# Kernel optimization log

Measured on AMD Instinct MI355X. Metric: run time of the kernel, lower is better.

Reference implementation:

```python
import jax, jax.numpy as jnp
import numpy as np

N, E = 50000, 800000          # nodes, edges
IN, H, OUT = 256, 128, 2       # input feat, hidden_channels, out_channels
NEG_SLOPE = 0.2                # GATv2 LeakyReLU slope (PyG default)


def _w(key, fan_in, fan_out):
    return jax.random.normal(key, (fan_in, fan_out), jnp.float32) / np.sqrt(fan_in).astype(np.float32)


def setup_inputs() -> dict:
    key = jax.random.key(0)
    ks = jax.random.split(key, 24)
    inp = {
        "x": jax.random.normal(ks[0], (N, IN), jnp.float32),
        "edge_index": jax.random.randint(ks[1], (2, E), 0, N, jnp.int32),
        # GATv2Conv 0: in=IN -> H
        "c0_Wl": _w(ks[2], IN, H), "c0_Wr": _w(ks[3], IN, H),
        "c0_att": jax.random.normal(ks[4], (H,), jnp.float32) / np.sqrt(H).astype(np.float32),
        "c0_b": jnp.zeros((H,), jnp.float32),
        # GATv2Conv 1: H -> H
        "c1_Wl": _w(ks[5], H, H), "c1_Wr": _w(ks[6], H, H),
        "c1_att": jax.random.normal(ks[7], (H,), jnp.float32) / np.sqrt(H).astype(np.float32),
        "c1_b": jnp.zeros((H,), jnp.float32),
        # final GATv2Conv: H -> OUT
        "cf_Wl": _w(ks[8], H, OUT), "cf_Wr": _w(ks[9], H, OUT),
        "cf_att": jax.random.normal(ks[10], (OUT,), jnp.float32) / np.sqrt(OUT).astype(np.float32),
        "cf_b": jnp.zeros((OUT,), jnp.float32),
        # residual Linears
        "l0_W": _w(ks[11], IN, H), "l0_b": jnp.zeros((H,), jnp.float32),
        "l1_W": _w(ks[12], H, H), "l1_b": jnp.zeros((H,), jnp.float32),
        "lf_W": _w(ks[13], H, OUT), "lf_b": jnp.zeros((OUT,), jnp.float32),
    }
    return inp


def gatv2(x, edge_index, Wl, Wr, att, bias):
    """PyG GATv2Conv, heads=1, add_self_loops=False, share_weights=False."""
    src, dst = edge_index[0], edge_index[1]
    xs = x @ Wl                                   # [N,H] source transform
    xd = x @ Wr                                   # [N,H] target transform
    h = jax.nn.leaky_relu(xs[src] + xd[dst], NEG_SLOPE)   # [E,H]
    e = h @ att                                   # [E] attention logits
    # segment softmax over incoming edges of each destination node
    m = jax.ops.segment_max(e, dst, num_segments=N)
    m = jnp.where(jnp.isfinite(m), m, 0.0)
    p = jnp.exp(e - m[dst])
    s = jax.ops.segment_sum(p, dst, num_segments=N)
    alpha = p / (s[dst] + 1e-16)                  # [E]
    out = jax.ops.segment_sum(alpha[:, None] * xs[src], dst, num_segments=N)
    return out + bias


def reference(x, edge_index, c0_Wl, c0_Wr, c0_att, c0_b, c1_Wl, c1_Wr, c1_att, c1_b,
              cf_Wl, cf_Wr, cf_att, cf_b, l0_W, l0_b, l1_W, l1_b, lf_W, lf_b):
    # layer 0 + residual linear, then ReLU
    h = gatv2(x, edge_index, c0_Wl, c0_Wr, c0_att, c0_b) + (jax.nn.relu(x) @ l0_W + l0_b)
    h = jax.nn.relu(h)
    # layer 1 -> embeddings
    emb = gatv2(h, edge_index, c1_Wl, c1_Wr, c1_att, c1_b) + (jax.nn.relu(h) @ l1_W + l1_b)
    # final layer -> logits
    out = gatv2(emb, edge_index, cf_Wl, cf_Wr, cf_att, cf_b) + (jax.nn.relu(emb) @ lf_W + lf_b)
    return (out, emb)
```

## Files before the change

kernel.cpp:

```cpp
#include <hip/hip_runtime.h>
#include <hip/hip_bf16.h>

#define NEG_SLOPE 0.2f

typedef __attribute__((ext_vector_type(8))) _Float16 half8;
typedef __attribute__((ext_vector_type(2))) _Float16 h2v;
typedef __attribute__((ext_vector_type(4))) float f32x4;

__device__ __forceinline__ float toF(float x) { return x; }
__device__ __forceinline__ float toF(__hip_bfloat16 x) { return __bfloat162float(x); }
__device__ __forceinline__ float toF(_Float16 x) { return (float)x; }

__device__ __forceinline__ void stT(float* p, size_t i, float v) { p[i] = v; }
__device__ __forceinline__ void stT(__hip_bfloat16* p, size_t i, float v) {
    p[i] = __float2bfloat16(v);
}
__device__ __forceinline__ void stT(_Float16* p, size_t i, float v) { p[i] = (_Float16)v; }

template <typename T> struct IsBF { static constexpr bool v = false; };
template <> struct IsBF<__hip_bfloat16> { static constexpr bool v = true; };

__device__ __forceinline__ void vwaitn(int n) {
    if (n == 0) asm volatile("s_waitcnt vmcnt(0)" ::: "memory");
    else if (n == 7) asm volatile("s_waitcnt vmcnt(7)" ::: "memory");
    else if (n == 8) asm volatile("s_waitcnt vmcnt(8)" ::: "memory");
    else if (n == 9) asm volatile("s_waitcnt vmcnt(9)" ::: "memory");
    else asm volatile("s_waitcnt vmcnt(10)" ::: "memory");
}

__global__ void k_detect(const unsigned* __restrict__ x, int* __restrict__ flag) {
    unsigned u = x[threadIdx.x];
    int lo_exp = (int)((u >> 7) & 0xFFu);
    int ok = (lo_exp >= 90 && lo_exp <= 141) ? 1 : 0;
    unsigned long long b = __ballot(ok);
    if (threadIdx.x == 0) flag[0] = (__popcll(b) >= 48) ? 1 : 0;
}

__global__ __launch_bounds__(256) void k_cnt(const int* __restrict__ src,
                                             const int* __restrict__ dst, int E,
                                             int* __restrict__ gcnt,
                                             unsigned* __restrict__ bbuf, int cap) {
    __shared__ int hist[64];
    __shared__ int lbase[64];
    __shared__ int gbase[64];
    __shared__ int lfill[64];
    __shared__ unsigned ebuf[4096];
    __shared__ unsigned char bb[4096];
    int t = threadIdx.x;
    int e0 = blockIdx.x * 4096;
    if (t < 64) { hist[t] = 0; lfill[t] = 0; }
    __syncthreads();
    unsigned my[16];
    int mybkt[16];
#pragma unroll
    for (int i = 0; i < 16; ++i) {
        int idx = e0 + i * 256 + t;
        if (idx < E) {
            int d = dst[idx];
            int b = d >> 10;
            mybkt[i] = b;
            my[i] = (unsigned)src[idx] | ((unsigned)(d & 1023) << 16);
            atomicAdd(&hist[b], 1);
        } else {
            mybkt[i] = -1;
        }
    }
    __syncthreads();
    if (t < 64) {
        int h = hist[t];
        int v = h;
#pragma unroll
        for (int o = 1; o < 64; o <<= 1) {
            int u = __shfl_up(v, o, 64);
            if (t >= o) v += u;
        }
        lbase[t] = v - h;
        gbase[t] = (h > 0) ? atomicAdd(&gcnt[t], h) : 0;
    }
    __syncthreads();
#pragma unroll
    for (int i = 0; i < 16; ++i) {
        int b = mybkt[i];
        if (b >= 0) {
            int p = lbase[b] + atomicAdd(&lfill[b], 1);
            ebuf[p] = my[i];
            bb[p] = (unsigned char)b;
        }
    }
    __syncthreads();
    int total = min(4096, E - e0);
    for (int p = t; p < total; p += 256) {
        int b = bb[p];
        int o = gbase[b] + (p - lbase[b]);
        if (o < cap) bbuf[(size_t)b * cap + o] = ebuf[p];
    }
}

__global__ void k_bbase(const int* __restrict__ gcnt, int* __restrict__ bbase, int nb,
                        int cap) {
    int t = threadIdx.x;
    int c = (t < nb) ? min(gcnt[t], cap) : 0;
    int v = c;
#pragma unroll
    for (int o = 1; o < 64; o <<= 1) {
        int u = __shfl_up(v, o, 64);
        if (t >= o) v += u;
    }
    if (t < nb) bbase[t] = v - c;
}

__global__ __launch_bounds__(256) void k_bhp(const int* __restrict__ gcnt,
                                             const int* __restrict__ bbase,
                                             const unsigned* __restrict__ bbuf, int cap,
                                             int* __restrict__ rowptr,
                                             int* __restrict__ csr_src, int n, int nb) {
    __shared__ int hist[1024];
    __shared__ int fill[1024];
    __shared__ int wsum[4];
    int b = blockIdx.x, t = threadIdx.x, lane = t & 63, w = t >> 6;
    for (int i = t; i < 1024; i += 256) { hist[i] = 0; fill[i] = 0; }
    __syncthreads();
    int cnt = min(gcnt[b], cap);
    const unsigned* p = bbuf + (size_t)b * cap;
    for (int i = t; i < cnt; i += 256) atomicAdd(&hist[p[i] >> 16], 1);
    __syncthreads();
    int base0 = bbase[b];
    int idx = t * 4;
    int c0 = hist[idx + 0], c1 = hist[idx + 1], c2 = hist[idx + 2], c3 = hist[idx + 3];
    int s1 = c0 + c1, s2 = s1 + c2, s3 = s2 + c3;
    int v = s3;
#pragma unroll
    for (int o = 1; o < 64; o <<= 1) {
        int u = __shfl_up(v, o, 64);
        if (lane >= o) v += u;
    }
    if (lane == 63) wsum[w] = v;
    __syncthreads();
    int woff = 0;
#pragma unroll
    for (int i = 0; i < 3; ++i)
        if (i < w) woff += wsum[i];
    int excl = base0 + woff + v - s3;
    hist[idx + 0] = excl;
    hist[idx + 1] = excl + c0;
    hist[idx + 2] = excl + s1;
    hist[idx + 3] = excl + s2;
    int d0 = b * 1024 + idx;
#pragma unroll
    for (int i = 0; i < 4; ++i)
        if (d0 + i < n) rowptr[d0 + i] = hist[idx + i];
    if (b == nb - 1 && t == 255) rowptr[n] = base0 + cnt;
    __syncthreads();
    for (int i = t; i < cnt; i += 256) {
        unsigned e = p[i];
        int dl = (int)(e >> 16);
        int pos = hist[dl] + atomicAdd(&fill[dl], 1);
        csr_src[pos] = (int)(e & 0xFFFFu);
    }
}

__global__ void k_hist(const int* __restrict__ dst, int E, int* __restrict__ rowptr) {
    int i = blockIdx.x * blockDim.x + threadIdx.x;
    if (i < E) atomicAdd(&rowptr[dst[i] + 1], 1);
}

__global__ void k_scatter(const int* __restrict__ src, const int* __restrict__ dst, int E,
                          const int* __restrict__ rowptr, int* __restrict__ fill,
                          int* __restrict__ csr_src) {
    int i = blockIdx.x * blockDim.x + threadIdx.x;
    if (i < E) {
        int d = dst[i];
        int pos = rowptr[d] + atomicAdd(&fill[d], 1);
        csr_src[pos] = src[i];
    }
}

__global__ __launch_bounds__(256) void k_scan1(int* __restrict__ rowptr,
                                               int* __restrict__ blksum, int n) {
    __shared__ int wsum[4];
    int t = threadIdx.x, lane = t & 63, w = t >> 6;
    int idx = blockIdx.x * 1024 + t * 4;
    int c0 = (idx + 0 < n) ? rowptr[idx + 1] : 0;
    int c1 = (idx + 1 < n) ? rowptr[idx + 2] : 0;
    int c2 = (idx + 2 < n) ? rowptr[idx + 3] : 0;
    int c3 = (idx + 3 < n) ? rowptr[idx + 4] : 0;
    int s1 = c0 + c1, s2 = s1 + c2, s3 = s2 + c3;
    int v = s3;
#pragma unroll
    for (int o = 1; o < 64; o <<= 1) {
        int u = __shfl_up(v, o, 64);
        if (lane >= o) v += u;
    }
    if (lane == 63) wsum[w] = v;
    __syncthreads();
    int woff = 0;
#pragma unroll
    for (int i = 0; i < 3; ++i)
        if (i < w) woff += wsum[i];
    int excl = woff + v - s3;
    if (idx + 0 < n) rowptr[idx + 1] = excl + c0;
    if (idx + 1 < n) rowptr[idx + 2] = excl + s1;
    if (idx + 2 < n) rowptr[idx + 3] = excl + s2;
    if (idx + 3 < n) rowptr[idx + 4] = excl + s3;
    if (t == 255) blksum[blockIdx.x] = woff + v;
}

__global__ void k_scan2(int* __restrict__ blksum, int nblk) {
    int t = threadIdx.x;
    int v = (t < nblk) ? blksum[t] : 0;
#pragma unroll
    for (int o = 1; o < 64; o <<= 1) {
        int u = __shfl_up(v, o, 64);
        if (t >= o) v += u;
    }
    if (t < nblk) blksum[t] = v;
}

__global__ void k_scan3(int* __restrict__ rowptr, const int* __restrict__ blksum, int n) {
    int idx = blockIdx.x * blockDim.x + threadIdx.x;
    if (idx < n) {
        int b = idx >> 10;
        if (b > 0) rowptr[idx + 1] += blksum[b - 1];
    }
}

template <typename WT>
__device__ void packW_body(const WT* W0, const WT* W1, const WT* W2, const WT* b2, int K,
                           _Float16* Bp, float* biasf) {
    int lane = threadIdx.x;
    int ksteps = K >> 5;
    int nb = 3 * ksteps * 8;
    int bid = blockIdx.x;
    if (bid == nb) {
        biasf[lane * 2 + 0] = toF(b2[lane * 2 + 0]);
        biasf[lane * 2 + 1] = toF(b2[lane * 2 + 1]);
        return;
    }
    int ks = bid / 24;
    int rem = bid - ks * 24;
    int o = rem >> 3, ct = rem & 7;
    const WT* W = (o == 0) ? W0 : ((o == 1) ? W1 : W2);
    int c = ct * 16 + (lane & 15);
    int k0 = ks * 32 + (lane >> 4) * 8;
    _Float16* out = Bp + (size_t)bid * 512 + lane * 8;
#pragma unroll
    for (int i = 0; i < 8; ++i) out[i] = (_Float16)toF(W[(size_t)(k0 + i) * 128 + c]);
}

__global__ void k_packW(const int* __restrict__ flag, const void* W0, const void* W1,
                        const void* W2, const void* b2, int K, _Float16* __restrict__ Bp,
                        float* __restrict__ biasf) {
    if (flag[0] == 0)
        packW_body<float>((const float*)W0, (const float*)W1, (const float*)W2,
                          (const float*)b2, K, Bp, biasf);
    else
        packW_body<__hip_bfloat16>((const __hip_bfloat16*)W0, (const __hip_bfloat16*)W1,
                                   (const __hip_bfloat16*)W2, (const __hip_bfloat16*)b2, K,
                                   Bp, biasf);
}

template <typename AT, typename O2T, int KSTEPS>
__device__ void gemm_body(const AT* __restrict__ A, int N,
                          const _Float16* __restrict__ Bp, const float* __restrict__ biasf,
                          _Float16* __restrict__ O0, _Float16* __restrict__ O1,
                          O2T* __restrict__ O2, _Float16 (*sB)[12288]) {
    const int H = 128;
    const int K = KSTEPS * 32;
    int tid = threadIdx.x;
    int wave = tid >> 6, lane = tid & 63;
    int row0 = (blockIdx.x * 4 + wave) * 16;
    int rr = lane & 15, kg = lane >> 4;
    int arow = min(row0 + rr, N - 1);
    constexpr int NR = (sizeof(AT) == 4) ? 2 : 1;

    f32x4 acc[3][8];
#pragma unroll
    for (int o = 0; o < 3; ++o)
#pragma unroll
        for (int ct = 0; ct < 8; ++ct) acc[o][ct] = f32x4{0.f, 0.f, 0.f, 0.f};

    auto stage = [&](int b, int ksv) {
        const char* gsrc = (const char*)(Bp + (size_t)ksv * 12288) + wave * 1024 + lane * 16;
        char* lbase = (char*)(&sB[b][0]) + wave * 1024;
#pragma unroll
        for (int r = 0; r < 6; ++r) {
            __builtin_amdgcn_global_load_lds(
                (const __attribute__((address_space(1))) unsigned*)(gsrc + r * 4096),
                (__attribute__((address_space(3))) unsigned*)(lbase + r * 4096), 16, 0, 0);
        }
    };
    auto loadA = [&](int ksv, uint4* dst) {
        const char* p = (const char*)A + ((size_t)arow * K + ksv * 32 + kg * 8) * sizeof(AT);
        dst[0] = *(const uint4*)p;
        if constexpr (NR == 2) dst[1] = *(const uint4*)(p + 16);
    };
    auto compute = [&](const uint4* raw, const _Float16* sb) {
        half8 a0, a1, r0f, r1f;
        if constexpr (sizeof(AT) == 4) {
            union { uint4 u[2]; float f[8]; } cv;
            cv.u[0] = raw[0]; cv.u[1] = raw[1];
#pragma unroll
            for (int i = 0; i < 8; ++i) {
                float a = cv.f[i];
                _Float16 h = (_Float16)a;
                float lof = a - (float)h;
                _Float16 lo = (_Float16)lof;
                bool pos = a > 0.f;
                a0[i] = h; a1[i] = lo;
                r0f[i] = pos ? h : (_Float16)0.f;
                r1f[i] = pos ? lo : (_Float16)0.f;
            }
        } else if constexpr (IsBF<AT>::v) {
            union { uint4 u4; unsigned u[4]; } cv;
            cv.u4 = raw[0];
#pragma unroll
            for (int q = 0; q < 4; ++q) {
                union { unsigned u; float f; } lo, hi;
                lo.u = cv.u[q] << 16;
                hi.u = cv.u[q] & 0xFFFF0000u;
                a0[2 * q] = (_Float16)lo.f;
                a0[2 * q + 1] = (_Float16)hi.f;
                r0f[2 * q] = (_Float16)fmaxf(lo.f, 0.f);
                r0f[2 * q + 1] = (_Float16)fmaxf(hi.f, 0.f);
            }
        } else {
            union { uint4 u4; half8 h; } cv;
            cv.u4 = raw[0];
            a0 = cv.h;
#pragma unroll
            for (int i = 0; i < 8; ++i)
                r0f[i] = (a0[i] > (_Float16)0.f) ? a0[i] : (_Float16)0.f;
        }
#pragma unroll
        for (int ct = 0; ct < 8; ++ct) {
            half8 w0 = *(const half8*)(sb + (0 * 8 + ct) * 512 + lane * 8);
            half8 w1 = *(const half8*)(sb + (1 * 8 + ct) * 512 + lane * 8);
            half8 w2 = *(const half8*)(sb + (2 * 8 + ct) * 512 + lane * 8);
            acc[0][ct] = __builtin_amdgcn_mfma_f32_16x16x32_f16(a0, w0, acc[0][ct], 0, 0, 0);
            acc[1][ct] = __builtin_amdgcn_mfma_f32_16x16x32_f16(a0, w1, acc[1][ct], 0, 0, 0);
            acc[2][ct] = __builtin_amdgcn_mfma_f32_16x16x32_f16(r0f, w2, acc[2][ct], 0, 0, 0);
            if constexpr (sizeof(AT) == 4) {
                acc[0][ct] = __builtin_amdgcn_mfma_f32_16x16x32_f16(a1, w0, acc[0][ct], 0, 0, 0);
                acc[1][ct] = __builtin_amdgcn_mfma_f32_16x16x32_f16(a1, w1, acc[1][ct], 0, 0, 0);
                acc[2][ct] = __builtin_amdgcn_mfma_f32_16x16x32_f16(r1f, w2, acc[2][ct], 0, 0, 0);
            }
        }
    };

    uint4 rA[3][NR];
    loadA(0, rA[0]);
    loadA(1, rA[1]);
    stage(0, 0);
#pragma unroll
    for (int ks = 0; ks < KSTEPS; ++ks) {
        if (ks + 1 < KSTEPS) {
            stage((ks + 1) & 1, ks + 1);
            asm volatile("" ::: "memory");
        }
        if (ks + 2 < KSTEPS) loadA(ks + 2, rA[(ks + 2) % 3]);
        if (ks == 0 || ks == KSTEPS - 2) vwaitn(NR + 6);
        else if (ks + 2 < KSTEPS) vwaitn(2 * NR + 6);
        else vwaitn(0);
        __builtin_amdgcn_s_barrier();
        compute(rA[ks % 3], &sB[ks & 1][0]);
        __builtin_amdgcn_s_barrier();
    }

    int rb = row0 + kg * 4;
#pragma unroll
    for (int ct = 0; ct < 8; ++ct) {
        int c = ct * 16 + rr;
        float bv = biasf[c];
#pragma unroll
        for (int j = 0; j < 4; ++j) {
            int row = rb + j;
            if (row < N) {
                size_t o = (size_t)row * H + c;
                O0[o] = (_Float16)acc[0][ct][j];
                O1[o] = (_Float16)acc[1][ct][j];
                stT(O2, o, acc[2][ct][j] + bv);
            }
        }
    }
}

template <int LAYER>
__global__ __launch_bounds__(256) void gemm3_u(const int* __restrict__ flag, const void* Aext,
                                               const _Float16* Af16, int N,
                                               const _Float16* __restrict__ Bp,
                                               const float* __restrict__ biasf,
                                               _Float16* __restrict__ O0,
                                               _Float16* __restrict__ O1, _Float16* O2h,
                                               float* O2f, __hip_bfloat16* O2b) {
    __shared__ _Float16 sB[2][12288];
    int f = flag[0];
    if constexpr (LAYER == 0) {
        if (f == 0)
            gemm_body<float, _Float16, 8>((const float*)Aext, N, Bp, biasf, O0, O1, O2h, sB);
        else
            gemm_body<__hip_bfloat16, _Float16, 8>((const __hip_bfloat16*)Aext, N, Bp, biasf,
                                                   O0, O1, O2h, sB);
    } else {
        if (f == 0)
            gemm_body<_Float16, float, 4>(Af16, N, Bp, biasf, O0, O1, O2f, sB);
        else
            gemm_body<_Float16, __hip_bfloat16, 4>(Af16, N, Bp, biasf, O0, O1, O2b, sB);
    }
}

template <typename IOT, typename T, int FINAL>
__device__ void gat_body(const _Float16* __restrict__ xs, const _Float16* __restrict__ xd,
                         const int* __restrict__ rowptr, const int* __restrict__ csr_src,
                         IOT* __restrict__ io, const T* __restrict__ att,
                         const T* __restrict__ gbias, int n, int relu_out,
                         const T* __restrict__ Wl, const T* __restrict__ Wr,
                         const T* __restrict__ Wres, const T* __restrict__ bres,
                         float* __restrict__ xsf, float* __restrict__ xdf,
                         float* __restrict__ resf) {
    int tid = threadIdx.x;
    int l = tid & 15;
    int g = tid >> 4;
    int dst = blockIdx.x * 16 + g;
    if (blockIdx.x * 16 + ((tid >> 6) << 2) >= n) return;
    int dstc = min(dst, n - 1);
    bool act = dst < n;

    union U4H { uint4 u; h2v h[4]; };
    U4H du; du.u = *(const uint4*)(xd + (size_t)dstc * 128 + l * 8);
    h2v ap[4];
#pragma unroll
    for (int c = 0; c < 4; ++c) {
        ap[c][0] = (_Float16)toF(att[l * 8 + 2 * c]);
        ap[c][1] = (_Float16)toF(att[l * 8 + 2 * c + 1]);
    }
    const _Float16 ks = (_Float16)NEG_SLOPE;
    const h2v k02 = {ks, ks};

    int beg = rowptr[dstc];
    int end = act ? rowptr[dstc + 1] : beg;
    float m = -INFINITY, s = 0.f;
    h2v acc[4];
#pragma unroll
    for (int c = 0; c < 4; ++c) acc[c] = h2v{(_Float16)0.f, (_Float16)0.f};

    auto GATHER = [&](U4H (&v)[8], int j0) {
#pragma unroll
        for (int q = 0; q < 8; ++q) {
            int idx = j0 + q;
            if (idx >= end) idx = j0;
            int sq = csr_src[idx];
            v[q].u = *(const uint4*)(xs + (size_t)sq * 128 + l * 8);
        }
    };
    auto COMPUTE = [&](U4H (&v)[8], int j0) {
        int rem = end - j0;
        float p[8];
#pragma unroll
        for (int q = 0; q < 8; ++q) p[q] = 0.f;
#pragma unroll
        for (int c = 0; c < 4; ++c) {
#pragma unroll
            for (int q = 0; q < 8; ++q) {
                h2v t = v[q].h[c] + du.h[c];
                t = __builtin_elementwise_max(t, t * k02);
                p[q] = __builtin_amdgcn_fdot2(t, ap[c], p[q], false);
            }
        }
#pragma unroll
        for (int o = 1; o < 16; o <<= 1) {
#pragma unroll
            for (int q = 0; q < 8; ++q) p[q] += __shfl_xor(p[q], o, 16);
        }
#pragma unroll
        for (int q = 1; q < 8; ++q)
            if (rem < q + 1) p[q] = -INFINITY;
        float pm = p[0];
#pragma unroll
        for (int q = 1; q < 8; ++q) pm = fmaxf(pm, p[q]);
        float nm = fmaxf(m, pm);
        float sc = __expf(m - nm);
        float w[8];
        float ws = 0.f;
#pragma unroll
        for (int q = 0; q < 8; ++q) {
            w[q] = __expf(p[q] - nm);
            ws += w[q];
        }
        s = s * sc + ws;
        _Float16 sch = (_Float16)sc;
        h2v scp = {sch, sch};
        h2v wp[8];
#pragma unroll
        for (int q = 0; q < 8; ++q) {
            _Float16 wh = (_Float16)w[q];
            wp[q] = h2v{wh, wh};
        }
#pragma unroll
        for (int c = 0; c < 4; ++c) {
            h2v a = acc[c] * scp;
#pragma unroll
            for (int q = 0; q < 8; ++q) a = a + v[q].h[c] * wp[q];
            acc[c] = a;
        }
        m = nm;
    };

    U4H va[8], vb[8];
    if (beg < end) GATHER(va, beg);
    for (int j = beg; j < end; j += 16) {
        if (j + 8 < end) GATHER(vb, j + 8);
        COMPUTE(va, j);
        if (j + 8 < end) {
            if (j + 16 < end) GATHER(va, j + 16);
            COMPUTE(vb, j + 8);
        }
    }

    if (act) {
        float r = 1.f / (s + 1e-16f);
        size_t base = (size_t)dst * 128 + l * 8;
        float ev[8];
#pragma unroll
        for (int c = 0; c < 4; ++c) {
            int f0 = l * 8 + 2 * c;
            float v0 = (float)acc[c][0] * r + toF(gbias[f0]) + toF(io[base + 2 * c]);
            float v1 = (float)acc[c][1] * r + toF(gbias[f0 + 1]) + toF(io[base + 2 * c + 1]);
            if (relu_out) { v0 = fmaxf(v0, 0.f); v1 = fmaxf(v1, 0.f); }
            stT(io, base + 2 * c, v0);
            stT(io, base + 2 * c + 1, v1);
            ev[2 * c] = v0;
            ev[2 * c + 1] = v1;
        }
        if constexpr (FINAL) {
            float d[6] = {0.f, 0.f, 0.f, 0.f, 0.f, 0.f};
#pragma unroll
            for (int f = 0; f < 8; ++f) {
                int fg = (l * 8 + f) * 2;
                float e = ev[f];
                float rp = fmaxf(e, 0.f);
                d[0] += e * toF(Wl[fg]);
                d[1] += e * toF(Wl[fg + 1]);
                d[2] += e * toF(Wr[fg]);
                d[3] += e * toF(Wr[fg + 1]);
                d[4] += rp * toF(Wres[fg]);
                d[5] += rp * toF(Wres[fg + 1]);
            }
#pragma unroll
            for (int i = 0; i < 6; ++i) {
#pragma unroll
                for (int o = 1; o < 16; o <<= 1) d[i] += __shfl_xor(d[i], o, 16);
            }
            if (l == 0) {
                xsf[dst * 2 + 0] = d[0];
                xsf[dst * 2 + 1] = d[1];
                xdf[dst * 2 + 0] = d[2];
                xdf[dst * 2 + 1] = d[3];
                resf[dst * 2 + 0] = d[4] + toF(bres[0]);
                resf[dst * 2 + 1] = d[5] + toF(bres[1]);
            }
        }
    }
}

template <int FINAL>
__global__ __launch_bounds__(256) void gat_u(const int* __restrict__ flag,
                                             const _Float16* __restrict__ xs,
                                             const _Float16* __restrict__ xd,
                                             const int* __restrict__ rowptr,
                                             const int* __restrict__ csr_src, _Float16* io_h,
                                             float* io_f, __hip_bfloat16* io_b, const void* att,
                                             const void* gbias, int n, int relu_out,
                                             const void* Wl, const void* Wr, const void* Wres,
                                             const void* bres, float* xsf, float* xdf,
                                             float* resf) {
    typedef __hip_bfloat16 bf;
    int f = flag[0];
    if constexpr (FINAL == 0) {
        if (f == 0)
            gat_body<_Float16, float, 0>(xs, xd, rowptr, csr_src, io_h, (const float*)att,
                                         (const float*)gbias, n, relu_out, nullptr, nullptr,
                                         nullptr, nullptr, nullptr, nullptr, nullptr);
        else
            gat_body<_Float16, bf, 0>(xs, xd, rowptr, csr_src, io_h, (const bf*)att,
                                      (const bf*)gbias, n, relu_out, nullptr, nullptr, nullptr,
                                      nullptr, nullptr, nullptr, nullptr);
    } else {
        if (f == 0)
            gat_body<float, float, 1>(xs, xd, rowptr, csr_src, io_f, (const float*)att,
                                      (const float*)gbias, n, relu_out, (const float*)Wl,
                                      (const float*)Wr, (const float*)Wres, (const float*)bres,
                                      xsf, xdf, resf);
        else
            gat_body<bf, bf, 1>(xs, xd, rowptr, csr_src, io_b, (const bf*)att, (const bf*)gbias,
                                n, relu_out, (const bf*)Wl, (const bf*)Wr, (const bf*)Wres,
                                (const bf*)bres, xsf, xdf, resf);
    }
}

template <typename T>
__device__ void fe_body(const float* __restrict__ xsf, const float* __restrict__ xdf,
                        const float* __restrict__ resf, const int* __restrict__ rowptr,
                        const int* __restrict__ csr_src, const T* __restrict__ att,
                        const T* __restrict__ gb, T* __restrict__ out, int n) {
    int dst = blockIdx.x * blockDim.x + threadIdx.x;
    if (dst >= n) return;
    float2 dv = ((const float2*)xdf)[dst];
    float a0 = toF(att[0]), a1 = toF(att[1]);
    float m = -INFINITY, s = 0.f, acc0 = 0.f, acc1 = 0.f;
    int beg = rowptr[dst], end = rowptr[dst + 1];
    for (int j = beg; j < end; j += 4) {
        int rem = end - j;
        int i1 = (rem > 1) ? 1 : 0, i2 = (rem > 2) ? 2 : 0, i3 = (rem > 3) ? 3 : 0;
        int s0 = csr_src[j];
        int s1 = csr_src[j + i1];
        int s2 = csr_src[j + i2];
        int s3 = csr_src[j + i3];
        float2 v0 = ((const float2*)xsf)[s0];
        float2 v1 = ((const float2*)xsf)[s1];
        float2 v2 = ((const float2*)xsf)[s2];
        float2 v3 = ((const float2*)xsf)[s3];
        float h0, h1, e0, e1, e2, e3;
        h0 = v0.x + dv.x; h0 = fmaxf(h0, NEG_SLOPE * h0);
        h1 = v0.y + dv.y; h1 = fmaxf(h1, NEG_SLOPE * h1);
        e0 = h0 * a0 + h1 * a1;
        h0 = v1.x + dv.x; h0 = fmaxf(h0, NEG_SLOPE * h0);
        h1 = v1.y + dv.y; h1 = fmaxf(h1, NEG_SLOPE * h1);
        e1 = h0 * a0 + h1 * a1;
        h0 = v2.x + dv.x; h0 = fmaxf(h0, NEG_SLOPE * h0);
        h1 = v2.y + dv.y; h1 = fmaxf(h1, NEG_SLOPE * h1);
        e2 = h0 * a0 + h1 * a1;
        h0 = v3.x + dv.x; h0 = fmaxf(h0, NEG_SLOPE * h0);
        h1 = v3.y + dv.y; h1 = fmaxf(h1, NEG_SLOPE * h1);
        e3 = h0 * a0 + h1 * a1;
        if (rem < 2) e1 = -INFINITY;
        if (rem < 3) e2 = -INFINITY;
        if (rem < 4) e3 = -INFINITY;
        float pm = fmaxf(fmaxf(e0, e1), fmaxf(e2, e3));
        float nm = fmaxf(m, pm);
        float sc = __expf(m - nm);
        float w0 = __expf(e0 - nm), w1 = __expf(e1 - nm);
        float w2 = __expf(e2 - nm), w3 = __expf(e3 - nm);
        s = s * sc + ((w0 + w1) + (w2 + w3));
        acc0 = acc0 * sc + ((w0 * v0.x + w1 * v1.x) + (w2 * v2.x + w3 * v3.x));
        acc1 = acc1 * sc + ((w0 * v0.y + w1 * v1.y) + (w2 * v2.y + w3 * v3.y));
        m = nm;
    }
    float r = 1.f / (s + 1e-16f);
    float2 rv = ((const float2*)resf)[dst];
    stT(out, (size_t)dst * 2 + 0, acc0 * r + toF(gb[0]) + rv.x);
    stT(out, (size_t)dst * 2 + 1, acc1 * r + toF(gb[1]) + rv.y);
}

__global__ void final_edge_u(const int* __restrict__ flag, const float* __restrict__ xsf,
                             const float* __restrict__ xdf, const float* __restrict__ resf,
                             const int* __restrict__ rowptr, const int* __restrict__ csr_src,
                             const void* att, const void* gb, void* out, int n) {
    typedef __hip_bfloat16 bf;
    if (flag[0] == 0)
        fe_body<float>(xsf, xdf, resf, rowptr, csr_src, (const float*)att, (const float*)gb,
                       (float*)out, n);
    else
        fe_body<bf>(xsf, xdf, resf, rowptr, csr_src, (const bf*)att, (const bf*)gb, (bf*)out, n);
}

extern "C" void kernel_launch(void* const* d_in, const int* in_sizes, int n_in,
                              void* d_out, int out_size, void* d_ws, size_t ws_size,
                              hipStream_t stream) {
    typedef __hip_bfloat16 bf;
    typedef _Float16 f16;
    const int IN = 256, H = 128;
    const int N = in_sizes[0] / IN;
    const int E = in_sizes[1] / 2;

    const int* ei = (const int*)d_in[1];

    size_t off = 0;
    auto alloc = [&](size_t bytes) {
        void* p = (char*)d_ws + off;
        off += (bytes + 255) & ~(size_t)255;
        return p;
    };
    f16* xs = (f16*)alloc((size_t)N * H * 2);
    f16* xd = (f16*)alloc((size_t)N * H * 2);
    f16* hb = (f16*)alloc((size_t)N * H * 2);
    int* flag = (int*)alloc(256);
    int* rowptr = (int*)alloc((size_t)(N + 1) * 4);
    int* fill = (int*)alloc((size_t)N * 4);
    int* blksum = (int*)alloc(256 * 4);
    int* csr_src = (int*)alloc((size_t)E * 4);
    float* xsf = (float*)alloc((size_t)N * 2 * 4);
    float* xdf = (float*)alloc((size_t)N * 2 * 4);
    float* resf = (float*)alloc((size_t)N * 2 * 4);
    f16* Bp0 = (f16*)alloc((size_t)3 * 8 * 8 * 512 * 2);
    f16* Bp1 = (f16*)alloc((size_t)3 * 4 * 8 * 512 * 2);
    float* bias0 = (float*)alloc(128 * 4);
    float* bias1 = (float*)alloc(128 * 4);
    const int NB = (N + 1023) / 1024;
    const int CAP = ((2 * (E / (NB > 0 ? NB : 1) + 1) + 255) / 256) * 256;
    int* gcnt = (int*)alloc(64 * 4);
    int* bbase = (int*)alloc(64 * 4);
    unsigned* bbuf = (unsigned*)alloc((size_t)NB * CAP * 4);

    const int* e_src = ei;
    const int* e_dst = ei + E;

    k_detect<<<1, 64, 0, stream>>>((const unsigned*)d_in[0], flag);
    if (N <= 65536) {
        hipMemsetAsync(gcnt, 0, 64 * 4, stream);
        k_cnt<<<(E + 4095) / 4096, 256, 0, stream>>>(e_src, e_dst, E, gcnt, bbuf, CAP);
        k_bbase<<<1, 64, 0, stream>>>(gcnt, bbase, NB, CAP);
        k_bhp<<<NB, 256, 0, stream>>>(gcnt, bbase, bbuf, CAP, rowptr, csr_src, N, NB);
    } else {
        const int nblk = (N + 1023) / 1024;
        hipMemsetAsync(rowptr, 0, (size_t)(N + 1) * 4, stream);
        hipMemsetAsync(fill, 0, (size_t)N * 4, stream);
        k_hist<<<(E + 255) / 256, 256, 0, stream>>>(e_dst, E, rowptr);
        k_scan1<<<nblk, 256, 0, stream>>>(rowptr, blksum, N);
        k_scan2<<<1, 64, 0, stream>>>(blksum, nblk);
        k_scan3<<<(N + 255) / 256, 256, 0, stream>>>(rowptr, blksum, N);
        k_scatter<<<(E + 255) / 256, 256, 0, stream>>>(e_src, e_dst, E, rowptr, fill, csr_src);
    }

    k_packW<<<3 * 8 * 8 + 1, 64, 0, stream>>>(flag, d_in[2], d_in[3], d_in[14], d_in[15], IN,
                                              Bp0, bias0);
    k_packW<<<3 * 4 * 8 + 1, 64, 0, stream>>>(flag, d_in[6], d_in[7], d_in[16], d_in[17], H,
                                              Bp1, bias1);

    const int g64 = (N + 63) / 64;
    const int eblk16 = (N + 15) / 16;

    float* embF = (float*)d_out + (size_t)N * 2;
    bf* embB = (bf*)d_out + (size_t)N * 2;

    gemm3_u<0><<<g64, 256, 0, stream>>>(flag, d_in[0], nullptr, N, Bp0, bias0, xs, xd, hb,
                                        nullptr, nullptr);
    gat_u<0><<<eblk16, 256, 0, stream>>>(flag, xs, xd, rowptr, csr_src, hb, nullptr, nullptr,
                                         d_in[4], d_in[5], N, 1, nullptr, nullptr, nullptr,
                                         nullptr, nullptr, nullptr, nullptr);

    gemm3_u<1><<<g64, 256, 0, stream>>>(flag, nullptr, hb, N, Bp1, bias1, xs, xd, nullptr,
                                        embF, embB);
    gat_u<1><<<eblk16, 256, 0, stream>>>(flag, xs, xd, rowptr, csr_src, nullptr, embF, embB,
                                         d_in[8], d_in[9], N, 0, d_in[10], d_in[11], d_in[18],
                                         d_in[19], xsf, xdf, resf);

    final_edge_u<<<(N + 255) / 256, 256, 0, stream>>>(flag, xsf, xdf, resf, rowptr, csr_src,
                                                      d_in[12], d_in[13], d_out, N);
}
```

Baseline: 325.0 us.

## Merge preprocessing launches and co-schedule edge bucketing with layer-0 GEMM

Merges dtype detection, gcnt zeroing and both weight-packing launches into one prep kernel. The edge bucket-count pass now runs in the same launch as the layer-0 GEMM (mega0), with blocks split by index. The bucket-base scan is folded into k_bhp, and the gather loop's double-buffered software pipeline is replaced by a simple single-buffer loop. The aim is fewer kernel launches and memset calls, plus overlapping CSR construction with GEMM work. Dropping the prefetch pipelining in the aggregation may expose more memory latency, and the shared 48KB dynamic shared memory can limit occupancy for the count blocks.

```diff
diff --git a/kernel.cpp b/kernel.cpp
--- a/kernel.cpp
+++ b/kernel.cpp
@@ -28,26 +28,82 @@
     else asm volatile("s_waitcnt vmcnt(10)" ::: "memory");
 }
 
-__global__ void k_detect(const unsigned* __restrict__ x, int* __restrict__ flag) {
-    unsigned u = x[threadIdx.x];
+__device__ __forceinline__ int detect_local(const unsigned* __restrict__ x, int t) {
+    unsigned u = x[t];
     int lo_exp = (int)((u >> 7) & 0xFFu);
     int ok = (lo_exp >= 90 && lo_exp <= 141) ? 1 : 0;
     unsigned long long b = __ballot(ok);
-    if (threadIdx.x == 0) flag[0] = (__popcll(b) >= 48) ? 1 : 0;
-}
-
-__global__ __launch_bounds__(256) void k_cnt(const int* __restrict__ src,
-                                             const int* __restrict__ dst, int E,
+    return (__popcll(b) >= 48) ? 1 : 0;
+}
+
+template <typename WT>
+__device__ void packW_body(const WT* W0, const WT* W1, const WT* W2, const WT* b2, int K,
+                           _Float16* Bp, float* biasf, int bid) {
+    int lane = threadIdx.x;
+    int ksteps = K >> 5;
+    int nb = 3 * ksteps * 8;
+    if (bid == nb) {
+        biasf[lane * 2 + 0] = toF(b2[lane * 2 + 0]);
+        biasf[lane * 2 + 1] = toF(b2[lane * 2 + 1]);
+        return;
+    }
+    int ks = bid / 24;
+    int rem = bid - ks * 24;
+    int o = rem >> 3, ct = rem & 7;
+    const WT* W = (o == 0) ? W0 : ((o == 1) ? W1 : W2);
+    int c = ct * 16 + (lane & 15);
+    int k0 = ks * 32 + (lane >> 4) * 8;
+    _Float16* out = Bp + (size_t)bid * 512 + lane * 8;
+#pragma unroll
+    for (int i = 0; i < 8; ++i) out[i] = (_Float16)toF(W[(size_t)(k0 + i) * 128 + c]);
+}
+
+__global__ __launch_bounds__(64) void k_prep(const unsigned* __restrict__ x, int* __restrict__ flag,
                                              int* __restrict__ gcnt,
-                                             unsigned* __restrict__ bbuf, int cap) {
-    __shared__ int hist[64];
-    __shared__ int lbase[64];
-    __shared__ int gbase[64];
-    __shared__ int lfill[64];
-    __shared__ unsigned ebuf[4096];
-    __shared__ unsigned char bb[4096];
+                                             const void* W0a, const void* W1a, const void* W2a,
+                                             const void* b2a, const void* W0b, const void* W1b,
+                                             const void* W2b, const void* b2b,
+                                             _Float16* __restrict__ Bp0, float* __restrict__ bias0,
+                                             _Float16* __restrict__ Bp1, float* __restrict__ bias1) {
+    typedef __hip_bfloat16 bf;
     int t = threadIdx.x;
-    int e0 = blockIdx.x * 4096;
+    int f = detect_local(x, t);
+    int bid = blockIdx.x;
+    if (bid == 0) {
+        if (t == 0) flag[0] = f;
+        gcnt[t] = 0;
+        return;
+    }
+    bid -= 1;
+    if (bid < 193) {
+        if (f == 0)
+            packW_body<float>((const float*)W0a, (const float*)W1a, (const float*)W2a,
+                              (const float*)b2a, 256, Bp0, bias0, bid);
+        else
+            packW_body<bf>((const bf*)W0a, (const bf*)W1a, (const bf*)W2a, (const bf*)b2a, 256,
+                           Bp0, bias0, bid);
+    } else {
+        bid -= 193;
+        if (f == 0)
+            packW_body<float>((const float*)W0b, (const float*)W1b, (const float*)W2b,
+                              (const float*)b2b, 128, Bp1, bias1, bid);
+        else
+            packW_body<bf>((const bf*)W0b, (const bf*)W1b, (const bf*)W2b, (const bf*)b2b, 128,
+                           Bp1, bias1, bid);
+    }
+}
+
+__device__ void k_cnt_body(const int* __restrict__ src, const int* __restrict__ dst, int E,
+                           int* __restrict__ gcnt, unsigned* __restrict__ bbuf, int cap,
+                           int bid, char* smem) {
+    int* hist = (int*)smem;
+    int* lbase = hist + 64;
+    int* gbase = lbase + 64;
+    int* lfill = gbase + 64;
+    unsigned* ebuf = (unsigned*)(lfill + 64);
+    unsigned char* bb = (unsigned char*)(ebuf + 4096);
+    int t = threadIdx.x;
+    int e0 = bid * 4096;
     if (t < 64) { hist[t] = 0; lfill[t] = 0; }
     __syncthreads();
     unsigned my[16];
@@ -96,35 +152,32 @@
     }
 }
 
-__global__ void k_bbase(const int* __restrict__ gcnt, int* __restrict__ bbase, int nb,
-                        int cap) {
-    int t = threadIdx.x;
-    int c = (t < nb) ? min(gcnt[t], cap) : 0;
-    int v = c;
-#pragma unroll
-    for (int o = 1; o < 64; o <<= 1) {
-        int u = __shfl_up(v, o, 64);
-        if (t >= o) v += u;
-    }
-    if (t < nb) bbase[t] = v - c;
-}
-
 __global__ __launch_bounds__(256) void k_bhp(const int* __restrict__ gcnt,
-                                             const int* __restrict__ bbase,
                                              const unsigned* __restrict__ bbuf, int cap,
                                              int* __restrict__ rowptr,
                                              int* __restrict__ csr_src, int n, int nb) {
     __shared__ int hist[1024];
     __shared__ int fill[1024];
     __shared__ int wsum[4];
+    __shared__ int bbs[64];
     int b = blockIdx.x, t = threadIdx.x, lane = t & 63, w = t >> 6;
     for (int i = t; i < 1024; i += 256) { hist[i] = 0; fill[i] = 0; }
-    __syncthreads();
+    if (t < 64) {
+        int c = (t < nb) ? min(gcnt[t], cap) : 0;
+        int v = c;
+#pragma unroll
+        for (int o = 1; o < 64; o <<= 1) {
+            int u = __shfl_up(v, o, 64);
+            if (t >= o) v += u;
+        }
+        bbs[t] = v;
+    }
+    __syncthreads();
+    int base0 = (b > 0) ? bbs[b - 1] : 0;
     int cnt = min(gcnt[b], cap);
     const unsigned* p = bbuf + (size_t)b * cap;
     for (int i = t; i < cnt; i += 256) atomicAdd(&hist[p[i] >> 16], 1);
     __syncthreads();
-    int base0 = bbase[b];
     int idx = t * 4;
     int c0 = hist[idx + 0], c1 = hist[idx + 1], c2 = hist[idx + 2], c3 = hist[idx + 3];
     int s1 = c0 + c1, s2 = s1 + c2, s3 = s2 + c3;
@@ -149,7 +202,7 @@
 #pragma unroll
     for (int i = 0; i < 4; ++i)
         if (d0 + i < n) rowptr[d0 + i] = hist[idx + i];
-    if (b == nb - 1 && t == 255) rowptr[n] = base0 + cnt;
+    if (b == nb - 1 && t == 255) rowptr[n] = bbs[nb - 1];
     __syncthreads();
     for (int i = t; i < cnt; i += 256) {
         unsigned e = p[i];
@@ -222,41 +275,6 @@
         int b = idx >> 10;
         if (b > 0) rowptr[idx + 1] += blksum[b - 1];
     }
-}
-
-template <typename WT>
-__device__ void packW_body(const WT* W0, const WT* W1, const WT* W2, const WT* b2, int K,
-                           _Float16* Bp, float* biasf) {
-    int lane = threadIdx.x;
-    int ksteps = K >> 5;
-    int nb = 3 * ksteps * 8;
-    int bid = blockIdx.x;
-    if (bid == nb) {
-        biasf[lane * 2 + 0] = toF(b2[lane * 2 + 0]);
-        biasf[lane * 2 + 1] = toF(b2[lane * 2 + 1]);
-        return;
-    }
-    int ks = bid / 24;
-    int rem = bid - ks * 24;
-    int o = rem >> 3, ct = rem & 7;
-    const WT* W = (o == 0) ? W0 : ((o == 1) ? W1 : W2);
-    int c = ct * 16 + (lane & 15);
-    int k0 = ks * 32 + (lane >> 4) * 8;
-    _Float16* out = Bp + (size_t)bid * 512 + lane * 8;
-#pragma unroll
-    for (int i = 0; i < 8; ++i) out[i] = (_Float16)toF(W[(size_t)(k0 + i) * 128 + c]);
-}
-
-__global__ void k_packW(const int* __restrict__ flag, const void* W0, const void* W1,
-                        const void* W2, const void* b2, int K, _Float16* __restrict__ Bp,
-                        float* __restrict__ biasf) {
-    if (flag[0] == 0)
-        packW_body<float>((const float*)W0, (const float*)W1, (const float*)W2,
-                          (const float*)b2, K, Bp, biasf);
-    else
-        packW_body<__hip_bfloat16>((const __hip_bfloat16*)W0, (const __hip_bfloat16*)W1,
-                                   (const __hip_bfloat16*)W2, (const __hip_bfloat16*)b2, K,
-                                   Bp, biasf);
 }
 
 template <typename AT, typename O2T, int KSTEPS>
@@ -381,6 +399,29 @@
                 stT(O2, o, acc[2][ct][j] + bv);
             }
         }
+    }
+}
+
+__global__ __launch_bounds__(256) void mega0(const int* __restrict__ flag, const void* Aext,
+                                             int N, int ngemm,
+                                             const _Float16* __restrict__ Bp0,
+                                             const float* __restrict__ bias0,
+                                             _Float16* __restrict__ xs, _Float16* __restrict__ xd,
+                                             _Float16* __restrict__ hb,
+                                             const int* __restrict__ e_src,
+                                             const int* __restrict__ e_dst, int E,
+                                             int* __restrict__ gcnt, unsigned* __restrict__ bbuf,
+                                             int cap) {
+    extern __shared__ char smem[];
+    if ((int)blockIdx.x < ngemm) {
+        auto sB = (_Float16(*)[12288])smem;
+        if (flag[0] == 0)
+            gemm_body<float, _Float16, 8>((const float*)Aext, N, Bp0, bias0, xs, xd, hb, sB);
+        else
+            gemm_body<__hip_bfloat16, _Float16, 8>((const __hip_bfloat16*)Aext, N, Bp0, bias0,
+                                                   xs, xd, hb, sB);
+    } else {
+        k_cnt_body(e_src, e_dst, E, gcnt, bbuf, cap, blockIdx.x - ngemm, smem);
     }
 }
 
@@ -443,17 +484,15 @@
 #pragma unroll
     for (int c = 0; c < 4; ++c) acc[c] = h2v{(_Float16)0.f, (_Float16)0.f};
 
-    auto GATHER = [&](U4H (&v)[8], int j0) {
+    for (int j = beg; j < end; j += 8) {
+        int rem = end - j;
+        U4H v[8];
 #pragma unroll
         for (int q = 0; q < 8; ++q) {
-            int idx = j0 + q;
-            if (idx >= end) idx = j0;
+            int idx = j + ((rem > q) ? q : 0);
             int sq = csr_src[idx];
             v[q].u = *(const uint4*)(xs + (size_t)sq * 128 + l * 8);
         }
-    };
-    auto COMPUTE = [&](U4H (&v)[8], int j0) {
-        int rem = end - j0;
         float p[8];
 #pragma unroll
         for (int q = 0; q < 8; ++q) p[q] = 0.f;
@@ -503,17 +542,6 @@
             acc[c] = a;
         }
         m = nm;
-    };
-
-    U4H va[8], vb[8];
-    if (beg < end) GATHER(va, beg);
-    for (int j = beg; j < end; j += 16) {
-        if (j + 8 < end) GATHER(vb, j + 8);
-        COMPUTE(va, j);
-        if (j + 8 < end) {
-            if (j + 16 < end) GATHER(va, j + 16);
-            COMPUTE(vb, j + 8);
-        }
     }
 
     if (act) {
@@ -698,18 +726,27 @@
     const int NB = (N + 1023) / 1024;
     const int CAP = ((2 * (E / (NB > 0 ? NB : 1) + 1) + 255) / 256) * 256;
     int* gcnt = (int*)alloc(64 * 4);
-    int* bbase = (int*)alloc(64 * 4);
     unsigned* bbuf = (unsigned*)alloc((size_t)NB * CAP * 4);
 
     const int* e_src = ei;
     const int* e_dst = ei + E;
 
-    k_detect<<<1, 64, 0, stream>>>((const unsigned*)d_in[0], flag);
+    k_prep<<<1 + 193 + 97, 64, 0, stream>>>((const unsigned*)d_in[0], flag, gcnt,
+                                            d_in[2], d_in[3], d_in[14], d_in[15],
+                                            d_in[6], d_in[7], d_in[16], d_in[17],
+                                            Bp0, bias0, Bp1, bias1);
+
+    const int g64 = (N + 63) / 64;
+    const int eblk16 = (N + 15) / 16;
+    const int ncnt = (E + 4095) / 4096;
+
+    float* embF = (float*)d_out + (size_t)N * 2;
+    bf* embB = (bf*)d_out + (size_t)N * 2;
+
     if (N <= 65536) {
-        hipMemsetAsync(gcnt, 0, 64 * 4, stream);
-        k_cnt<<<(E + 4095) / 4096, 256, 0, stream>>>(e_src, e_dst, E, gcnt, bbuf, CAP);
-        k_bbase<<<1, 64, 0, stream>>>(gcnt, bbase, NB, CAP);
-        k_bhp<<<NB, 256, 0, stream>>>(gcnt, bbase, bbuf, CAP, rowptr, csr_src, N, NB);
+        mega0<<<g64 + ncnt, 256, 49152, stream>>>(flag, d_in[0], N, g64, Bp0, bias0, xs, xd,
+                                                  hb, e_src, e_dst, E, gcnt, bbuf, CAP);
+        k_bhp<<<NB, 256, 0, stream>>>(gcnt, bbuf, CAP, rowptr, csr_src, N, NB);
     } else {
         const int nblk = (N + 1023) / 1024;
         hipMemsetAsync(rowptr, 0, (size_t)(N + 1) * 4, stream);
@@ -719,21 +756,10 @@
         k_scan2<<<1, 64, 0, stream>>>(blksum, nblk);
         k_scan3<<<(N + 255) / 256, 256, 0, stream>>>(rowptr, blksum, N);
         k_scatter<<<(E + 255) / 256, 256, 0, stream>>>(e_src, e_dst, E, rowptr, fill, csr_src);
-    }
-
-    k_packW<<<3 * 8 * 8 + 1, 64, 0, stream>>>(flag, d_in[2], d_in[3], d_in[14], d_in[15], IN,
-                                              Bp0, bias0);
-    k_packW<<<3 * 4 * 8 + 1, 64, 0, stream>>>(flag, d_in[6], d_in[7], d_in[16], d_in[17], H,
-                                              Bp1, bias1);
-
-    const int g64 = (N + 63) / 64;
-    const int eblk16 = (N + 15) / 16;
-
-    float* embF = (float*)d_out + (size_t)N * 2;
-    bf* embB = (bf*)d_out + (size_t)N * 2;
-
-    gemm3_u<0><<<g64, 256, 0, stream>>>(flag, d_in[0], nullptr, N, Bp0, bias0, xs, xd, hb,
-                                        nullptr, nullptr);
+        gemm3_u<0><<<g64, 256, 0, stream>>>(flag, d_in[0], nullptr, N, Bp0, bias0, xs, xd, hb,
+                                            nullptr, nullptr);
+    }
+
     gat_u<0><<<eblk16, 256, 0, stream>>>(flag, xs, xd, rowptr, csr_src, hb, nullptr, nullptr,
                                          d_in[4], d_in[5], N, 1, nullptr, nullptr, nullptr,
                                          nullptr, nullptr, nullptr, nullptr);
```

Result: slower. 353.4 us (+8.8%).
